# Kernel tuning notes

Measured on AMD Instinct MI355X. Metric: run time of the kernel, lower is better.

Reference implementation:

```python
import jax, jax.numpy as jnp
import numpy as np

NPART = 128
NSTART = 128
NEND = 128
BATCH = 4096


def setup_inputs() -> dict:
    key = jax.random.key(0)
    k1, k2, k3, k4, k5 = jax.random.split(key, 5)
    gaussian = jax.random.normal(k1, (BATCH, NSTART), dtype=jnp.float32)
    logp = jax.random.normal(k2, (NPART, 1), dtype=jnp.float32)
    pos = 3.0 * jax.random.normal(k3, (NPART, NSTART), dtype=jnp.float32)
    sigma = 0.1 * jax.random.normal(k4, (NPART, NEND, NEND), dtype=jnp.float32)
    # deterministic stand-in for tf.random.categorical(logp.T, batch)
    randind = jax.random.randint(k5, (BATCH,), 0, NPART, dtype=jnp.int32)
    return {"gaussian": gaussian, "logp": logp, "pos": pos,
            "sigma": sigma, "randind": randind}


def reference(gaussian, logp, pos, sigma, randind):
    batch = gaussian.shape[0]
    y = gaussian.reshape(batch, -1)                      # [B, nend]
    p = jax.nn.softmax(logp[:, 0], axis=0)               # [npart]
    weights = p[randind]                                 # [B]
    pos_g = pos[randind]                                 # [B, nstart]
    # full per-particle matmul as in the original: [npart, B, nend]
    temp = jnp.einsum('pij,bj->pbi', sigma, y)
    vv = temp[randind, jnp.arange(batch)]                # gather one particle per sample -> [B, nend]
    out = (pos_g + vv).reshape(gaussian.shape)
    return out, weights, randind
```

## Files before the change

kernel.cpp:

```cpp
#include <hip/hip_runtime.h>

#define NPART 128
#define NDIM  128
#define BATCH 4096
#define BPP   4
#define NBLK  (NPART * BPP)
#define NXCD  8

__global__ __launch_bounds__(256)
void mix_kernel(const float* __restrict__ gaussian,
                const float* __restrict__ logp,
                const float* __restrict__ pos,
                const float* __restrict__ sigma,
                const int*   __restrict__ randind,
                float* __restrict__ out,
                float* __restrict__ wout,
                float* __restrict__ indout) {
    const int g  = blockIdx.x;
    const int sg = (g % NXCD) * (NBLK / NXCD) + g / NXCD;
    const int p  = sg >> 2;
    const int q  = sg & 3;
    const int t  = threadIdx.x;
    const int i  = t & 127;
    const int hf = t >> 7;
    const int lane = t & 63, wid = t >> 6;

    __shared__ float4 smat[NDIM * 32];
    __shared__ int    wtot[4];
    __shared__ int    slist[160];
    __shared__ float  smx[2];

    const int4* rnd4 = reinterpret_cast<const int4*>(randind);
    int mk[16];
    {
        int4 a = rnd4[t * 4 + 0], b = rnd4[t * 4 + 1],
             c = rnd4[t * 4 + 2], d = rnd4[t * 4 + 3];
        mk[0]=a.x;  mk[1]=a.y;  mk[2]=a.z;  mk[3]=a.w;
        mk[4]=b.x;  mk[5]=b.y;  mk[6]=b.z;  mk[7]=b.w;
        mk[8]=c.x;  mk[9]=c.y;  mk[10]=c.z; mk[11]=c.w;
        mk[12]=d.x; mk[13]=d.y; mk[14]=d.z; mk[15]=d.w;
    }

    if (t < 64) {
        float a = logp[t], b = logp[t + 64];
        float m = fmaxf(a, b);
        #pragma unroll
        for (int o = 32; o > 0; o >>= 1) m = fmaxf(m, __shfl_xor(m, o));
        float ea = expf(a - m), eb = expf(b - m);
        float s = ea + eb;
        #pragma unroll
        for (int o = 32; o > 0; o >>= 1) s += __shfl_xor(s, o);
        if (t == 0) { smx[0] = m; smx[1] = s; }
    }

    int cnt = 0;
    #pragma unroll
    for (int k = 0; k < 16; ++k) cnt += (mk[k] == p) ? 1 : 0;
    int v = cnt;
    #pragma unroll
    for (int o = 1; o < 64; o <<= 1) {
        int u = __shfl_up(v, o);
        if (lane >= o) v += u;
    }
    if (lane == 63) wtot[wid] = v;
    __syncthreads();
    int woff = 0;
    #pragma unroll
    for (int w = 0; w < 4; ++w) woff += (w < wid) ? wtot[w] : 0;
    const int base = woff + v - cnt;
    const int n    = wtot[0] + wtot[1] + wtot[2] + wtot[3];
    const int lo   = (n * q) / BPP;
    const int hi   = (n * (q + 1)) / BPP;
    const int nq   = hi - lo;
    {
        int r = base;
        #pragma unroll
        for (int k = 0; k < 16; ++k) {
            if (mk[k] == p) {
                if (r >= lo && r < hi) slist[r - lo] = t * 16 + k;
                ++r;
            }
        }
    }
    if (nq == 0) return;

    const float4* src = reinterpret_cast<const float4*>(
        sigma + (size_t)p * NDIM * NDIM);
    #pragma unroll
    for (int w = 0; w < 16; ++w) {
        int idx = w * 256 + t;
        int r = idx >> 5, u = idx & 31;
        smat[r * 32 + (u ^ (r & 7))] = src[idx];
    }
    __syncthreads();

    float4 sr[32];
    #pragma unroll
    for (int u = 0; u < 32; ++u)
        sr[u] = smat[i * 32 + (u ^ (i & 7))];

    const float posv = pos[p * NDIM + i];
    const float pw   = expf(logp[p] - smx[0]) / smx[1];

    for (int s = hf; s < nq; s += 2) {
        const int sid = __builtin_amdgcn_readfirstlane(slist[s]);
        const float4* y = reinterpret_cast<const float4*>(
            gaussian + (size_t)sid * NDIM);
        float a0 = 0.f, a1 = 0.f, a2 = 0.f, a3 = 0.f;
        #pragma unroll
        for (int u = 0; u < 32; ++u) {
            float4 yv = y[u];
            float4 sv = sr[u];
            a0 += sv.x * yv.x;  a1 += sv.y * yv.y;
            a2 += sv.z * yv.z;  a3 += sv.w * yv.w;
        }
        out[sid * NDIM + i] = posv + ((a0 + a1) + (a2 + a3));
        if (i == 0) {
            wout[sid]   = pw;
            indout[sid] = (float)p;
        }
    }
}

extern "C" void kernel_launch(void* const* d_in, const int* in_sizes, int n_in,
                              void* d_out, int out_size, void* d_ws, size_t ws_size,
                              hipStream_t stream) {
    const float* gaussian = (const float*)d_in[0];
    const float* logp     = (const float*)d_in[1];
    const float* pos      = (const float*)d_in[2];
    const float* sigma    = (const float*)d_in[3];
    const int*   randind  = (const int*)d_in[4];

    float* out    = (float*)d_out;
    float* wout   = out + BATCH * NDIM;
    float* indout = wout + BATCH;

    mix_kernel<<<NBLK, 256, 0, stream>>>(gaussian, logp, pos, sigma, randind,
                                         out, wout, indout);
}
```

Before: 16.03 us.

## Split sigma rows across wave halves, load directly to registers, drop LDS staging

Removes the 64KB shared-memory staging of the sigma matrix. Each thread now loads half a row (16 float4) straight from global memory into registers, and the two halves are combined with a cross-lane shuffle. Every sample is processed by all 256 threads instead of alternating between two 128-thread halves. This cuts LDS use and register pressure, which should raise occupancy, at the cost of uncoalesced strided row loads and an extra shuffle per output.

```diff
diff --git a/kernel.cpp b/kernel.cpp
--- a/kernel.cpp
+++ b/kernel.cpp
@@ -21,14 +21,13 @@
     const int p  = sg >> 2;
     const int q  = sg & 3;
     const int t  = threadIdx.x;
-    const int i  = t & 127;
-    const int hf = t >> 7;
     const int lane = t & 63, wid = t >> 6;
+    const int row  = wid * 32 + (lane & 31);
+    const int half = lane >> 5;
 
-    __shared__ float4 smat[NDIM * 32];
-    __shared__ int    wtot[4];
-    __shared__ int    slist[160];
-    __shared__ float  smx[2];
+    __shared__ int   wtot[4];
+    __shared__ int   slist[160];
+    __shared__ float smx[2];
 
     const int4* rnd4 = reinterpret_cast<const int4*>(randind);
     int mk[16];
@@ -72,50 +71,45 @@
     const int lo   = (n * q) / BPP;
     const int hi   = (n * (q + 1)) / BPP;
     const int nq   = hi - lo;
+    if (nq == 0) return;
+
+    const float4* srow = reinterpret_cast<const float4*>(
+        sigma + (size_t)p * NDIM * NDIM + row * NDIM + half * 64);
+    float4 sr[16];
+    #pragma unroll
+    for (int u = 0; u < 16; ++u) sr[u] = srow[u];
+
+    const float pw = expf(logp[p] - smx[0]) / smx[1];
     {
         int r = base;
         #pragma unroll
         for (int k = 0; k < 16; ++k) {
             if (mk[k] == p) {
-                if (r >= lo && r < hi) slist[r - lo] = t * 16 + k;
+                if (r >= lo && r < hi && (r - lo) < 160) slist[r - lo] = t * 16 + k;
                 ++r;
             }
         }
     }
-    if (nq == 0) return;
-
-    const float4* src = reinterpret_cast<const float4*>(
-        sigma + (size_t)p * NDIM * NDIM);
-    #pragma unroll
-    for (int w = 0; w < 16; ++w) {
-        int idx = w * 256 + t;
-        int r = idx >> 5, u = idx & 31;
-        smat[r * 32 + (u ^ (r & 7))] = src[idx];
-    }
+    const float posv = pos[p * NDIM + row];
     __syncthreads();
 
-    float4 sr[32];
-    #pragma unroll
-    for (int u = 0; u < 32; ++u)
-        sr[u] = smat[i * 32 + (u ^ (i & 7))];
-
-    const float posv = pos[p * NDIM + i];
-    const float pw   = expf(logp[p] - smx[0]) / smx[1];
-
-    for (int s = hf; s < nq; s += 2) {
-        const int sid = __builtin_amdgcn_readfirstlane(slist[s]);
+    for (int s = 0; s < nq; ++s) {
+        const int sid = slist[s];
         const float4* y = reinterpret_cast<const float4*>(
-            gaussian + (size_t)sid * NDIM);
+            gaussian + (size_t)sid * NDIM + half * 64);
         float a0 = 0.f, a1 = 0.f, a2 = 0.f, a3 = 0.f;
         #pragma unroll
-        for (int u = 0; u < 32; ++u) {
+        for (int u = 0; u < 16; ++u) {
             float4 yv = y[u];
             float4 sv = sr[u];
             a0 += sv.x * yv.x;  a1 += sv.y * yv.y;
             a2 += sv.z * yv.z;  a3 += sv.w * yv.w;
         }
-        out[sid * NDIM + i] = posv + ((a0 + a1) + (a2 + a3));
-        if (i == 0) {
+        float part = (a0 + a1) + (a2 + a3);
+        float tot  = part + __shfl_xor(part, 32);
+        if (half == 0)
+            out[sid * NDIM + row] = posv + tot;
+        if (t == 0) {
             wout[sid]   = pw;
             indout[sid] = (float)p;
         }
```

Measured after the change: 22.14 us. 1.38x slower.

## Store sigma rows as packed fp16 and use fdot2 for the matvec

Applied to the files above, without the earlier changes.

Sigma is converted to packed half pairs on load and kept in a half-size LDS tile. Each thread holds its row in half the registers, and the dot product uses v_dot2 fp16 instructions with fp32 accumulation, with the gaussian input converted to fp16 on the fly. The early exit moves ahead of the slist fill and the launch bounds add an occupancy hint. This lowers register and LDS pressure and the instruction count, but inputs are rounded to fp16, which costs accuracy.

```diff
diff --git a/kernel.cpp b/kernel.cpp
--- a/kernel.cpp
+++ b/kernel.cpp
@@ -7,7 +7,9 @@
 #define NBLK  (NPART * BPP)
 #define NXCD  8
 
-__global__ __launch_bounds__(256)
+typedef __fp16 half2v __attribute__((ext_vector_type(2)));
+
+__global__ __launch_bounds__(256, 4)
 void mix_kernel(const float* __restrict__ gaussian,
                 const float* __restrict__ logp,
                 const float* __restrict__ pos,
@@ -25,7 +27,7 @@
     const int hf = t >> 7;
     const int lane = t & 63, wid = t >> 6;
 
-    __shared__ float4 smat[NDIM * 32];
+    __shared__ float4 tile16[NDIM * 16];
     __shared__ int    wtot[4];
     __shared__ int    slist[160];
     __shared__ float  smx[2];
@@ -72,6 +74,9 @@
     const int lo   = (n * q) / BPP;
     const int hi   = (n * (q + 1)) / BPP;
     const int nq   = hi - lo;
+    if (nq == 0) return;
+
+    const float pw = expf(logp[p] - smx[0]) / smx[1];
     {
         int r = base;
         #pragma unroll
@@ -82,25 +87,44 @@
             }
         }
     }
-    if (nq == 0) return;
 
-    const float4* src = reinterpret_cast<const float4*>(
-        sigma + (size_t)p * NDIM * NDIM);
-    #pragma unroll
-    for (int w = 0; w < 16; ++w) {
-        int idx = w * 256 + t;
-        int r = idx >> 5, u = idx & 31;
-        smat[r * 32 + (u ^ (r & 7))] = src[idx];
+    {
+        const float4* src = reinterpret_cast<const float4*>(
+            sigma + (size_t)p * NDIM * NDIM);
+        float4 stg[16];
+        #pragma unroll
+        for (int w = 0; w < 8; ++w) {
+            stg[2 * w]     = src[w * 512 + 2 * t];
+            stg[2 * w + 1] = src[w * 512 + 2 * t + 1];
+        }
+        #pragma unroll
+        for (int w = 0; w < 8; ++w) {
+            half2v h0 = __builtin_amdgcn_cvt_pkrtz(stg[2*w].x,   stg[2*w].y);
+            half2v h1 = __builtin_amdgcn_cvt_pkrtz(stg[2*w].z,   stg[2*w].w);
+            half2v h2 = __builtin_amdgcn_cvt_pkrtz(stg[2*w+1].x, stg[2*w+1].y);
+            half2v h3 = __builtin_amdgcn_cvt_pkrtz(stg[2*w+1].z, stg[2*w+1].w);
+            float4 o;
+            o.x = __builtin_bit_cast(float, h0);
+            o.y = __builtin_bit_cast(float, h1);
+            o.z = __builtin_bit_cast(float, h2);
+            o.w = __builtin_bit_cast(float, h3);
+            const int slot = w * 256 + t;
+            const int r = slot >> 4, u = slot & 15;
+            tile16[r * 16 + (u ^ (r & 15))] = o;
+        }
     }
+    const float posv = pos[p * NDIM + i];
     __syncthreads();
 
-    float4 sr[32];
+    half2v srh[64];
     #pragma unroll
-    for (int u = 0; u < 32; ++u)
-        sr[u] = smat[i * 32 + (u ^ (i & 7))];
-
-    const float posv = pos[p * NDIM + i];
-    const float pw   = expf(logp[p] - smx[0]) / smx[1];
+    for (int u = 0; u < 16; ++u) {
+        float4 tmp = tile16[i * 16 + (u ^ (i & 15))];
+        srh[4*u+0] = __builtin_bit_cast(half2v, tmp.x);
+        srh[4*u+1] = __builtin_bit_cast(half2v, tmp.y);
+        srh[4*u+2] = __builtin_bit_cast(half2v, tmp.z);
+        srh[4*u+3] = __builtin_bit_cast(half2v, tmp.w);
+    }
 
     for (int s = hf; s < nq; s += 2) {
         const int sid = __builtin_amdgcn_readfirstlane(slist[s]);
@@ -108,11 +132,17 @@
             gaussian + (size_t)sid * NDIM);
         float a0 = 0.f, a1 = 0.f, a2 = 0.f, a3 = 0.f;
         #pragma unroll
-        for (int u = 0; u < 32; ++u) {
-            float4 yv = y[u];
-            float4 sv = sr[u];
-            a0 += sv.x * yv.x;  a1 += sv.y * yv.y;
-            a2 += sv.z * yv.z;  a3 += sv.w * yv.w;
+        for (int jj = 0; jj < 32; ++jj) {
+            float4 yv = y[jj];
+            half2v h0 = __builtin_amdgcn_cvt_pkrtz(yv.x, yv.y);
+            half2v h1 = __builtin_amdgcn_cvt_pkrtz(yv.z, yv.w);
+            if (jj & 1) {
+                a2 = __builtin_amdgcn_fdot2(srh[2*jj],   h0, a2, false);
+                a3 = __builtin_amdgcn_fdot2(srh[2*jj+1], h1, a3, false);
+            } else {
+                a0 = __builtin_amdgcn_fdot2(srh[2*jj],   h0, a0, false);
+                a1 = __builtin_amdgcn_fdot2(srh[2*jj+1], h1, a1, false);
+            }
         }
         out[sid * NDIM + i] = posv + ((a0 + a1) + (a2 + a3));
         if (i == 0) {
```

Result: no change. 16.03 us (-0.0%).
